# Optimization experiments

Measured on AMD Instinct MI355X. Metric: run time of the kernel, lower is better.

Reference implementation:

```python
import jax, jax.numpy as jnp
from jax import lax
import numpy as np

D = 4      # agent_state_vector_length
H = 32     # hidden width (hardcoded in module)
N = 128    # agents
T = 100    # timesteps


def setup_inputs() -> dict:
    key = jax.random.key(0)
    ks = jax.random.split(key, 16)
    g = lambda k, s: jax.random.normal(k, s, dtype=jnp.float32) * 0.05
    return {
        "x": jax.random.normal(ks[0], (N, T, D), dtype=jnp.float32),
        # Conv1d weights stored [out_ch, in_ch, k] (OIH)
        "w1": g(ks[1], (16, D, 3)), "b1": g(ks[2], (16,)),
        "w2": g(ks[3], (32, 16, 3)), "b2": g(ks[4], (32,)),
        "w3": g(ks[5], (32, 32, 3)), "b3": g(ks[6], (32,)),
        # Linear weights stored [in, out]
        "We": g(ks[7], (2 * H, H)), "be": g(ks[8], (H,)),
        "Wa": g(ks[9], (H, H)),     "ba": g(ks[10], (H,)),
        "Wu": g(ks[11], (2 * H, H)), "bu": g(ks[12], (H,)),
        "Wd": g(ks[13], (H, D)),    "bd": g(ks[14], (D,)),
    }


def _forward(x, w1, b1, w2, b2, w3, b3, We, be, Wa, ba, Wu, bu, Wd, bd):
    # ---- conv_1d: per-agent temporal encoder (agents batched) ----
    h = jnp.transpose(x, (0, 2, 1))  # [N, D, T]
    def conv(h, w, b):
        y = lax.conv_general_dilated(h, w, (1,), 'VALID',
                                     dimension_numbers=('NCH', 'OIH', 'NCH'))
        return jax.nn.relu(y + b[None, :, None])
    h = conv(h, w1, b1)
    h = conv(h, w2, b2)
    h = conv(h, w3, b3)            # [N, H, T-6]
    h = jnp.transpose(h, (2, 0, 1))  # [T', N, H]  (time_steps)
    Tp = h.shape[0]

    # ---- graph_conv: all-pairs edge MLP + sum aggregation (j != i) ----
    Wj, Wi = We[:H], We[H:]          # concat(node_j, node_i) split
    ej = jnp.einsum('tjc,cd->tjd', h, Wj)  # sender part
    ei = jnp.einsum('tic,cd->tid', h, Wi)  # receiver part
    e = jax.nn.relu(ej[:, None, :, :] + ei[:, :, None, :] + be)  # [T',i,j,H]
    diag = jax.nn.relu(ej + ei + be)       # i == j terms, excluded by loop
    agg = e.sum(axis=2) - diag             # [T', N, H]
    agg = jax.nn.relu(agg @ Wa + ba)
    upd = jax.nn.relu(h @ Wu[:H] + agg @ Wu[H:] + bu)  # concat(node_i, agg)

    # ---- decode: residual over original state at t+6 ----
    dec = upd @ Wd + bd                    # [T', N, D]
    out = x[:, 6:6 + Tp] + jnp.transpose(dec, (1, 0, 2))  # [N, T', D]
    return out


def reference(x, w1, b1, w2, b2, w3, b3, We, be, Wa, ba, Wu, bu, Wd, bd):
    return _forward(x, w1, b1, w2, b2, w3, b3, We, be, Wa, ba, Wu, bu, Wd, bd)
```

## Files before the change

### kernel.cpp

```cpp
#include <hip/hip_runtime.h>


#define NN 128
#define TT 100
#define TP 94
#define HH 32

__global__ __launch_bounds__(256) void k_conv(
    const float* __restrict__ x,
    const float* __restrict__ w1, const float* __restrict__ b1,
    const float* __restrict__ w2, const float* __restrict__ b2,
    const float* __restrict__ w3, const float* __restrict__ b3,
    const float* __restrict__ We,
    float* __restrict__ h_g, float* __restrict__ ej_g, float* __restrict__ ei_g)
{
    __shared__ float sx[4][56];
    __shared__ float s1[16][56];
    __shared__ float s2[32][56];
    __shared__ float s3[32][48];

    const int n    = blockIdx.x;
    const int half = blockIdx.y;
    const int t0g  = half * 46;
    const int tid  = threadIdx.x;

    if (tid < 54) {
        float4 v = ((const float4*)x)[n * TT + t0g + tid];
        sx[0][tid] = v.x; sx[1][tid] = v.y; sx[2][tid] = v.z; sx[3][tid] = v.w;
    }
    if (tid >= 64 && tid < 128) {
        int r = tid - 64;
        s1[r >> 2][52 + (r & 3)] = 0.f;
    }
    __syncthreads();

    for (int idx = tid; idx < 16 * 52; idx += 256) {
        int o = idx / 52, t = idx - o * 52;
        float acc = b1[o];
        #pragma unroll
        for (int i = 0; i < 4; ++i)
            #pragma unroll
            for (int k = 0; k < 3; ++k)
                acc += sx[i][t + k] * w1[o * 12 + i * 3 + k];
        s1[o][t] = fmaxf(acc, 0.f);
    }
    __syncthreads();

    {
        const int op = tid & 15, seg = tid >> 4;
        if (seg < 13) {
            const int t0 = seg * 4;
            float acc0[4], acc1[4];
            float bv0 = b2[op], bv1 = b2[op + 16];
            #pragma unroll
            for (int u = 0; u < 4; ++u) { acc0[u] = bv0; acc1[u] = bv1; }
            #pragma unroll
            for (int i = 0; i < 16; ++i) {
                float4 f0 = *(const float4*)&s1[i][t0];
                float4 f1 = *(const float4*)&s1[i][t0 + 4];
                float a[6] = {f0.x, f0.y, f0.z, f0.w, f1.x, f1.y};
                float W00 = w2[op * 48 + i * 3 + 0];
                float W01 = w2[op * 48 + i * 3 + 1];
                float W02 = w2[op * 48 + i * 3 + 2];
                float W10 = w2[(op + 16) * 48 + i * 3 + 0];
                float W11 = w2[(op + 16) * 48 + i * 3 + 1];
                float W12 = w2[(op + 16) * 48 + i * 3 + 2];
                #pragma unroll
                for (int u = 0; u < 4; ++u) {
                    acc0[u] += a[u] * W00 + a[u + 1] * W01 + a[u + 2] * W02;
                    acc1[u] += a[u] * W10 + a[u + 1] * W11 + a[u + 2] * W12;
                }
            }
            #pragma unroll
            for (int u = 0; u < 4; ++u) {
                s2[op][t0 + u]      = fmaxf(acc0[u], 0.f);
                s2[op + 16][t0 + u] = fmaxf(acc1[u], 0.f);
            }
        }
    }
    __syncthreads();

    {
        const int op = tid & 15, seg = tid >> 4;
        if (seg < 12) {
            const int t0 = seg * 4;
            float acc0[4], acc1[4];
            float bv0 = b3[op], bv1 = b3[op + 16];
            #pragma unroll
            for (int u = 0; u < 4; ++u) { acc0[u] = bv0; acc1[u] = bv1; }
            #pragma unroll
            for (int i = 0; i < 32; ++i) {
                float4 f0 = *(const float4*)&s2[i][t0];
                float4 f1 = *(const float4*)&s2[i][t0 + 4];
                float a[6] = {f0.x, f0.y, f0.z, f0.w, f1.x, f1.y};
                float W00 = w3[op * 96 + i * 3 + 0];
                float W01 = w3[op * 96 + i * 3 + 1];
                float W02 = w3[op * 96 + i * 3 + 2];
                float W10 = w3[(op + 16) * 96 + i * 3 + 0];
                float W11 = w3[(op + 16) * 96 + i * 3 + 1];
                float W12 = w3[(op + 16) * 96 + i * 3 + 2];
                #pragma unroll
                for (int u = 0; u < 4; ++u) {
                    acc0[u] += a[u] * W00 + a[u + 1] * W01 + a[u + 2] * W02;
                    acc1[u] += a[u] * W10 + a[u + 1] * W11 + a[u + 2] * W12;
                }
            }
            #pragma unroll
            for (int u = 0; u < 4; ++u) {
                float v0 = fmaxf(acc0[u], 0.f);
                float v1 = fmaxf(acc1[u], 0.f);
                s3[op][t0 + u]      = v0;
                s3[op + 16][t0 + u] = v1;
                int tg = t0g + t0 + u;
                h_g[(tg * NN + n) * HH + op]      = v0;
                h_g[(tg * NN + n) * HH + op + 16] = v1;
            }
        }
    }
    __syncthreads();

    {
        const int dp = tid & 15, seg = tid >> 4;
        if (seg < 12) {
            const int t0 = seg * 4;
            float aj0[4], ai0[4], aj1[4], ai1[4];
            #pragma unroll
            for (int u = 0; u < 4; ++u) { aj0[u]=0.f; ai0[u]=0.f; aj1[u]=0.f; ai1[u]=0.f; }
            #pragma unroll
            for (int c = 0; c < 32; ++c) {
                float4 f0 = *(const float4*)&s3[c][t0];
                float hv[4] = {f0.x, f0.y, f0.z, f0.w};
                float wj0 = We[c * 32 + dp];
                float wj1 = We[c * 32 + dp + 16];
                float wi0 = We[(32 + c) * 32 + dp];
                float wi1 = We[(32 + c) * 32 + dp + 16];
                #pragma unroll
                for (int u = 0; u < 4; ++u) {
                    aj0[u] += hv[u] * wj0;
                    aj1[u] += hv[u] * wj1;
                    ai0[u] += hv[u] * wi0;
                    ai1[u] += hv[u] * wi1;
                }
            }
            #pragma unroll
            for (int u = 0; u < 4; ++u) {
                int tg = t0g + t0 + u;
                ej_g[(tg * NN + n) * HH + dp]      = aj0[u];
                ej_g[(tg * NN + n) * HH + dp + 16] = aj1[u];
                ei_g[(tg * NN + n) * HH + dp]      = ai0[u];
                ei_g[(tg * NN + n) * HH + dp + 16] = ai1[u];
            }
        }
    }
}

__global__ __launch_bounds__(256) void k_agg(
    const float* __restrict__ x,
    const float* __restrict__ h_g, const float* __restrict__ ej_g,
    const float* __restrict__ ei_g,
    const float* __restrict__ be, const float* __restrict__ Wa,
    const float* __restrict__ ba, const float* __restrict__ Wu,
    const float* __restrict__ bu, const float* __restrict__ Wd,
    const float* __restrict__ bd, float* __restrict__ out)
{
    const int t  = blockIdx.x;
    const int ib = blockIdx.y;
    const int tid = threadIdx.x;

    __shared__ float sej[NN * HH];
    __shared__ float sei[32 * HH];
    __shared__ float sh[32 * HH];
    __shared__ float sagg[32 * HH];
    __shared__ float sagg2[32 * HH];
    __shared__ float supd[32 * HH];

    {
        const float4* ej4 = (const float4*)(ej_g + t * NN * HH);
        float4* s4 = (float4*)sej;
        #pragma unroll
        for (int u = 0; u < 4; ++u) s4[tid + 256 * u] = ej4[tid + 256 * u];
        const float4* ei4 = (const float4*)(ei_g + (t * NN + ib * 32) * HH);
        const float4* h4  = (const float4*)(h_g  + (t * NN + ib * 32) * HH);
        ((float4*)sei)[tid] = ei4[tid];
        ((float4*)sh)[tid]  = h4[tid];
    }
    __syncthreads();

    const int d  = tid & 31;
    const int i0 = tid >> 5;

    {
        float bev = be[d];
        float c[4], acc[4];
        #pragma unroll
        for (int u = 0; u < 4; ++u) {
            int i = i0 + u * 8;
            c[u] = sei[i * HH + d] + bev;
            acc[u] = -fmaxf(sej[(ib * 32 + i) * HH + d] + c[u], 0.f);
        }
        #pragma unroll 8
        for (int j = 0; j < NN; ++j) {
            float v = sej[j * HH + d];
            #pragma unroll
            for (int u = 0; u < 4; ++u)
                acc[u] += fmaxf(v + c[u], 0.f);
        }
        #pragma unroll
        for (int u = 0; u < 4; ++u)
            sagg[(i0 + u * 8) * HH + d] = acc[u];
    }
    __syncthreads();

    {
        float acc[4];
        float bav = ba[d];
        #pragma unroll
        for (int u = 0; u < 4; ++u) acc[u] = bav;
        #pragma unroll
        for (int c = 0; c < 32; ++c) {
            float wa = Wa[c * 32 + d];
            #pragma unroll
            for (int u = 0; u < 4; ++u)
                acc[u] += sagg[(i0 + u * 8) * HH + c] * wa;
        }
        #pragma unroll
        for (int u = 0; u < 4; ++u)
            sagg2[(i0 + u * 8) * HH + d] = fmaxf(acc[u], 0.f);
    }
    __syncthreads();

    {
        float acc[4];
        float buv = bu[d];
        #pragma unroll
        for (int u = 0; u < 4; ++u) acc[u] = buv;
        #pragma unroll
        for (int c = 0; c < 32; ++c) {
            float wh = Wu[c * 32 + d];
            float wg = Wu[(32 + c) * 32 + d];
            #pragma unroll
            for (int u = 0; u < 4; ++u) {
                int i = i0 + u * 8;
                acc[u] += sh[i * HH + c] * wh + sagg2[i * HH + c] * wg;
            }
        }
        #pragma unroll
        for (int u = 0; u < 4; ++u)
            supd[(i0 + u * 8) * HH + d] = fmaxf(acc[u], 0.f);
    }
    __syncthreads();

    if (tid < 128) {
        int i = tid >> 2, d4 = tid & 3;
        int n = ib * 32 + i;
        float a = bd[d4];
        #pragma unroll
        for (int c = 0; c < 32; ++c)
            a += supd[i * HH + c] * Wd[c * 4 + d4];
        out[n * (TP * 4) + t * 4 + d4] = x[n * (TT * 4) + (6 + t) * 4 + d4] + a;
    }
}

extern "C" void kernel_launch(void* const* d_in, const int* in_sizes, int n_in,
                              void* d_out, int out_size, void* d_ws, size_t ws_size,
                              hipStream_t stream) {
    const float* x  = (const float*)d_in[0];
    const float* w1 = (const float*)d_in[1];
    const float* b1 = (const float*)d_in[2];
    const float* w2 = (const float*)d_in[3];
    const float* b2 = (const float*)d_in[4];
    const float* w3 = (const float*)d_in[5];
    const float* b3 = (const float*)d_in[6];
    const float* We = (const float*)d_in[7];
    const float* be = (const float*)d_in[8];
    const float* Wa = (const float*)d_in[9];
    const float* ba = (const float*)d_in[10];
    const float* Wu = (const float*)d_in[11];
    const float* bu = (const float*)d_in[12];
    const float* Wd = (const float*)d_in[13];
    const float* bd = (const float*)d_in[14];

    float* ws   = (float*)d_ws;
    float* h_g  = ws;
    float* ej_g = ws + TP * NN * HH;
    float* ei_g = ws + 2 * TP * NN * HH;

    k_conv<<<dim3(NN, 2), 256, 0, stream>>>(x, w1, b1, w2, b2, w3, b3, We,
                                            h_g, ej_g, ei_g);
    k_agg<<<dim3(TP, 4), 256, 0, stream>>>(x, h_g, ej_g, ei_g,
                                           be, Wa, ba, Wu, bu, Wd, bd,
                                           (float*)d_out);
}
```

Measured before the change: 105.1 us.

## Double agents per agg block, read ej from global, vectorize small matmuls

The aggregation kernel now handles 64 receiving agents per block instead of 32, so each thread keeps 8 accumulators and the grid halves to 188 blocks. It no longer stages ej, ei and h in shared memory and reads them straight from global/L2. The Wa and Wu matmuls are recast so each thread computes a float4 of outputs for two agents, using float4 loads of weights and activations, and all 256 threads now take part in the decode. The aim is to cut shared-memory staging, the extra sync and redundant ej loads per block. The cost is fewer blocks to fill the GPU and more global-memory traffic in the inner j-loop.

Result: slower. 109.6 us (+4.3%).

```diff
diff --git a/kernel.cpp b/kernel.cpp
--- a/kernel.cpp
+++ b/kernel.cpp
@@ -154,6 +154,11 @@
     }
 }
 
+__device__ __forceinline__ float4 relu4(float4 v) {
+    return make_float4(fmaxf(v.x, 0.f), fmaxf(v.y, 0.f),
+                       fmaxf(v.z, 0.f), fmaxf(v.w, 0.f));
+}
+
 __global__ __launch_bounds__(256) void k_agg(
     const float* __restrict__ x,
     const float* __restrict__ h_g, const float* __restrict__ ej_g,
@@ -163,100 +168,118 @@
     const float* __restrict__ bu, const float* __restrict__ Wd,
     const float* __restrict__ bd, float* __restrict__ out)
 {
-    const int t  = blockIdx.x;
-    const int ib = blockIdx.y;
+    const int t   = blockIdx.x;
+    const int ib  = blockIdx.y;
     const int tid = threadIdx.x;
 
-    __shared__ float sej[NN * HH];
-    __shared__ float sei[32 * HH];
-    __shared__ float sh[32 * HH];
-    __shared__ float sagg[32 * HH];
-    __shared__ float sagg2[32 * HH];
-    __shared__ float supd[32 * HH];
-
-    {
-        const float4* ej4 = (const float4*)(ej_g + t * NN * HH);
-        float4* s4 = (float4*)sej;
-        #pragma unroll
-        for (int u = 0; u < 4; ++u) s4[tid + 256 * u] = ej4[tid + 256 * u];
-        const float4* ei4 = (const float4*)(ei_g + (t * NN + ib * 32) * HH);
-        const float4* h4  = (const float4*)(h_g  + (t * NN + ib * 32) * HH);
-        ((float4*)sei)[tid] = ei4[tid];
-        ((float4*)sh)[tid]  = h4[tid];
-    }
-    __syncthreads();
-
-    const int d  = tid & 31;
-    const int i0 = tid >> 5;
-
-    {
+    __shared__ float sagg[64 * HH];
+    __shared__ float sagg2[64 * HH];
+    __shared__ float supd[64 * HH];
+
+    const float* ejt = ej_g + t * NN * HH;
+    const float* eit = ei_g + (t * NN + ib * 64) * HH;
+    const float* ht  = h_g  + (t * NN + ib * 64) * HH;
+
+    {
+        const int d  = tid & 31;
+        const int i0 = tid >> 5;
         float bev = be[d];
-        float c[4], acc[4];
-        #pragma unroll
-        for (int u = 0; u < 4; ++u) {
-            int i = i0 + u * 8;
-            c[u] = sei[i * HH + d] + bev;
-            acc[u] = -fmaxf(sej[(ib * 32 + i) * HH + d] + c[u], 0.f);
-        }
-        #pragma unroll 8
+        float c[8], acc[8];
+        #pragma unroll
+        for (int u = 0; u < 8; ++u) {
+            int il = i0 + u * 8;
+            c[u] = eit[il * HH + d] + bev;
+            acc[u] = -fmaxf(ejt[(ib * 64 + il) * HH + d] + c[u], 0.f);
+        }
+        #pragma unroll 4
         for (int j = 0; j < NN; ++j) {
-            float v = sej[j * HH + d];
-            #pragma unroll
-            for (int u = 0; u < 4; ++u)
+            float v = ejt[j * HH + d];
+            #pragma unroll
+            for (int u = 0; u < 8; ++u)
                 acc[u] += fmaxf(v + c[u], 0.f);
         }
         #pragma unroll
-        for (int u = 0; u < 4; ++u)
+        for (int u = 0; u < 8; ++u)
             sagg[(i0 + u * 8) * HH + d] = acc[u];
     }
     __syncthreads();
 
-    {
-        float acc[4];
-        float bav = ba[d];
-        #pragma unroll
-        for (int u = 0; u < 4; ++u) acc[u] = bav;
-        #pragma unroll
-        for (int c = 0; c < 32; ++c) {
-            float wa = Wa[c * 32 + d];
-            #pragma unroll
-            for (int u = 0; u < 4; ++u)
-                acc[u] += sagg[(i0 + u * 8) * HH + c] * wa;
-        }
-        #pragma unroll
-        for (int u = 0; u < 4; ++u)
-            sagg2[(i0 + u * 8) * HH + d] = fmaxf(acc[u], 0.f);
-    }
-    __syncthreads();
-
-    {
-        float acc[4];
-        float buv = bu[d];
-        #pragma unroll
-        for (int u = 0; u < 4; ++u) acc[u] = buv;
-        #pragma unroll
-        for (int c = 0; c < 32; ++c) {
-            float wh = Wu[c * 32 + d];
-            float wg = Wu[(32 + c) * 32 + d];
-            #pragma unroll
-            for (int u = 0; u < 4; ++u) {
-                int i = i0 + u * 8;
-                acc[u] += sh[i * HH + c] * wh + sagg2[i * HH + c] * wg;
-            }
-        }
-        #pragma unroll
-        for (int u = 0; u < 4; ++u)
-            supd[(i0 + u * 8) * HH + d] = fmaxf(acc[u], 0.f);
-    }
-    __syncthreads();
-
-    if (tid < 128) {
-        int i = tid >> 2, d4 = tid & 3;
-        int n = ib * 32 + i;
+    const int dg = tid & 7;
+    const int ii = tid >> 3;
+    {
+        const float4* Wa4 = (const float4*)Wa;
+        const float4* sagg4 = (const float4*)sagg;
+        float4 bav = ((const float4*)ba)[dg];
+        float4 accA = bav, accB = bav;
+        #pragma unroll
+        for (int c4 = 0; c4 < 8; ++c4) {
+            float4 aA = sagg4[ii * 8 + c4];
+            float4 aB = sagg4[(ii + 32) * 8 + c4];
+            float vA[4] = {aA.x, aA.y, aA.z, aA.w};
+            float vB[4] = {aB.x, aB.y, aB.z, aB.w};
+            #pragma unroll
+            for (int m = 0; m < 4; ++m) {
+                float4 w = Wa4[(c4 * 4 + m) * 8 + dg];
+                accA.x += vA[m] * w.x; accA.y += vA[m] * w.y;
+                accA.z += vA[m] * w.z; accA.w += vA[m] * w.w;
+                accB.x += vB[m] * w.x; accB.y += vB[m] * w.y;
+                accB.z += vB[m] * w.z; accB.w += vB[m] * w.w;
+            }
+        }
+        ((float4*)sagg2)[ii * 8 + dg]        = relu4(accA);
+        ((float4*)sagg2)[(ii + 32) * 8 + dg] = relu4(accB);
+    }
+    __syncthreads();
+
+    {
+        const float4* Wu4 = (const float4*)Wu;
+        const float4* h4  = (const float4*)ht;
+        const float4* g4  = (const float4*)sagg2;
+        float4 buv = ((const float4*)bu)[dg];
+        float4 accA = buv, accB = buv;
+        #pragma unroll
+        for (int c4 = 0; c4 < 8; ++c4) {
+            float4 hA = h4[ii * 8 + c4];
+            float4 hB = h4[(ii + 32) * 8 + c4];
+            float4 gA = g4[ii * 8 + c4];
+            float4 gB = g4[(ii + 32) * 8 + c4];
+            float vhA[4] = {hA.x, hA.y, hA.z, hA.w};
+            float vhB[4] = {hB.x, hB.y, hB.z, hB.w};
+            float vgA[4] = {gA.x, gA.y, gA.z, gA.w};
+            float vgB[4] = {gB.x, gB.y, gB.z, gB.w};
+            #pragma unroll
+            for (int m = 0; m < 4; ++m) {
+                float4 wh = Wu4[(c4 * 4 + m) * 8 + dg];
+                float4 wg = Wu4[(32 + c4 * 4 + m) * 8 + dg];
+                accA.x += vhA[m] * wh.x + vgA[m] * wg.x;
+                accA.y += vhA[m] * wh.y + vgA[m] * wg.y;
+                accA.z += vhA[m] * wh.z + vgA[m] * wg.z;
+                accA.w += vhA[m] * wh.w + vgA[m] * wg.w;
+                accB.x += vhB[m] * wh.x + vgB[m] * wg.x;
+                accB.y += vhB[m] * wh.y + vgB[m] * wg.y;
+                accB.z += vhB[m] * wh.z + vgB[m] * wg.z;
+                accB.w += vhB[m] * wh.w + vgB[m] * wg.w;
+            }
+        }
+        ((float4*)supd)[ii * 8 + dg]        = relu4(accA);
+        ((float4*)supd)[(ii + 32) * 8 + dg] = relu4(accB);
+    }
+    __syncthreads();
+
+    {
+        const int i  = tid >> 2;
+        const int d4 = tid & 3;
+        const float4* supd4 = (const float4*)supd;
         float a = bd[d4];
         #pragma unroll
-        for (int c = 0; c < 32; ++c)
-            a += supd[i * HH + c] * Wd[c * 4 + d4];
+        for (int c4 = 0; c4 < 8; ++c4) {
+            float4 uu = supd4[i * 8 + c4];
+            float vu[4] = {uu.x, uu.y, uu.z, uu.w};
+            #pragma unroll
+            for (int m = 0; m < 4; ++m)
+                a += vu[m] * Wd[(c4 * 4 + m) * 4 + d4];
+        }
+        int n = ib * 64 + i;
         out[n * (TP * 4) + t * 4 + d4] = x[n * (TT * 4) + (6 + t) * 4 + d4] + a;
     }
 }
@@ -287,7 +310,7 @@
 
     k_conv<<<dim3(NN, 2), 256, 0, stream>>>(x, w1, b1, w2, b2, w3, b3, We,
                                             h_g, ej_g, ei_g);
-    k_agg<<<dim3(TP, 4), 256, 0, stream>>>(x, h_g, ej_g, ei_g,
+    k_agg<<<dim3(TP, 2), 256, 0, stream>>>(x, h_g, ej_g, ei_g,
                                            be, Wa, ba, Wu, bu, Wd, bd,
                                            (float*)d_out);
 }
```
